# Performance work log

Hardware: AMD Instinct MI355X
Metric: run time of the kernel (lower is better)

## Reference

```python
import jax, jax.numpy as jnp
import numpy as np

B, T, I, U, O, BB = 256, 1024, 64, 256, 64, 128  # batch, seq, input, units, output, backbone_units

def lecun_tanh(x):
    return 1.7159 * jnp.tanh(0.666 * x)

def setup_inputs() -> dict:
    key = jax.random.key(0)
    ks = jax.random.split(key, 13)
    def lin(k, fan_in, fan_out):
        bound = 1.0 / np.sqrt(fan_in)
        kw, kb = jax.random.split(k)
        W = jax.random.uniform(kw, (fan_in, fan_out), jnp.float32, -bound, bound)
        b = jax.random.uniform(kb, (fan_out,), jnp.float32, -bound, bound)
        return W, b
    x = jax.random.normal(ks[0], (B, T, I), jnp.float32)
    W_bb, b_bb = lin(ks[1], I + U, BB)   # backbone Linear
    W_ff1, b_ff1 = lin(ks[2], BB, U)
    W_ff2, b_ff2 = lin(ks[3], BB, U)
    W_ta, b_ta = lin(ks[4], BB, U)       # time_a
    W_tb, b_tb = lin(ks[5], BB, U)       # time_b
    W_fc, b_fc = lin(ks[6], U, O)        # readout
    return {"x": x, "W_bb": W_bb, "b_bb": b_bb, "W_ff1": W_ff1, "b_ff1": b_ff1,
            "W_ff2": W_ff2, "b_ff2": b_ff2, "W_ta": W_ta, "b_ta": b_ta,
            "W_tb": W_tb, "b_tb": b_tb, "W_fc": W_fc, "b_fc": b_fc}

def reference(x, W_bb, b_bb, W_ff1, b_ff1, W_ff2, b_ff2, W_ta, b_ta, W_tb, b_tb, W_fc, b_fc):
    ts = jnp.float32(1.0)  # default elapsed time per step
    def step(h, xt):
        z = jnp.concatenate([xt, h], axis=-1)          # [B, I+U]
        g = lecun_tanh(z @ W_bb + b_bb)                # [B, BB]
        ff1 = jnp.tanh(g @ W_ff1 + b_ff1)              # [B, U]
        ff2 = jnp.tanh(g @ W_ff2 + b_ff2)
        t_interp = jax.nn.sigmoid((g @ W_ta + b_ta) * ts + (g @ W_tb + b_tb))
        h_new = ff1 * (1.0 - t_interp) + t_interp * ff2
        return h_new, h_new
    h0 = jnp.zeros((x.shape[0], U), x.dtype)
    h_last, hs = jax.lax.scan(step, h0, jnp.swapaxes(x, 0, 1))  # hs: [T, B, U]
    hs = jnp.swapaxes(hs, 0, 1)                                  # [B, T, U]
    out = hs @ W_fc + b_fc                                       # [B, T, O]
    return out, h_last
```

## Files before the change

### kernel.cpp

```cpp
#include <hip/hip_runtime.h>
#include <stdint.h>

#define B_ 256
#define T_ 1024
#define I_ 64
#define U_ 256
#define O_ 64
#define BB_ 128

typedef unsigned int u32;
typedef unsigned short u16;
typedef _Float16 half2_t __attribute__((ext_vector_type(2)));
typedef _Float16 f16x8 __attribute__((ext_vector_type(8)));
typedef float f32x4 __attribute__((ext_vector_type(4)));

#if defined(__has_builtin)
#if __has_builtin(__builtin_amdgcn_fdot2)
#define USE_DOT2 1
#else
#define USE_DOT2 0
#endif
#else
#define USE_DOT2 0
#endif

static __device__ __forceinline__ u32 packpair(float a, float b) {
  half2_t h; h.x = (_Float16)a; h.y = (_Float16)b;
  return __builtin_bit_cast(u32, h);
}
#if defined(__has_builtin) && __has_builtin(__builtin_amdgcn_cvt_pkrtz)
static __device__ __forceinline__ u32 pkrtz(float a, float b) {
  return __builtin_bit_cast(u32, __builtin_amdgcn_cvt_pkrtz(a, b));
}
#else
static __device__ __forceinline__ u32 pkrtz(float a, float b) {
  return packpair(a, b);
}
#endif
static __device__ __forceinline__ float unpack_lo(u32 u) {
  half2_t h = __builtin_bit_cast(half2_t, u); return (float)h.x;
}
static __device__ __forceinline__ float unpack_hi(u32 u) {
  half2_t h = __builtin_bit_cast(half2_t, u); return (float)h.y;
}
static __device__ __forceinline__ float dot2acc(u32 w, u32 z, float acc) {
#if USE_DOT2
  return __builtin_amdgcn_fdot2(__builtin_bit_cast(half2_t, w),
                                __builtin_bit_cast(half2_t, z), acc, false);
#else
  half2_t hw = __builtin_bit_cast(half2_t, w);
  half2_t hz = __builtin_bit_cast(half2_t, z);
  acc += (float)hw.x * (float)hz.x;
  acc += (float)hw.y * (float)hz.y;
  return acc;
#endif
}

template <int CTRL>
static __device__ __forceinline__ float dpp_mov_f(float v) {
  return __builtin_bit_cast(float, __builtin_amdgcn_update_dpp(
      0, __builtin_bit_cast(int, v), CTRL, 0xF, 0xF, true));
}
#define DPP_XOR1 0xB1
#define DPP_XOR2 0x4E
#define DPP_HMIR 0x141
#define DPP_MIRR 0x140

static __device__ __forceinline__ float fast_tanh(float x) {
  return 1.0f - 2.0f / (1.0f + __expf(2.0f * x));
}
static __device__ __forceinline__ float fast_sigmoid(float x) {
  return 1.0f / (1.0f + __expf(-x));
}

static __device__ __forceinline__ float rcpf(float x) {
#if defined(__has_builtin) && __has_builtin(__builtin_amdgcn_rcpf)
  return __builtin_amdgcn_rcpf(x);
#else
  return 1.0f / x;
#endif
}
static __device__ __forceinline__ float exp2fast(float x) {
#if defined(__has_builtin) && __has_builtin(__builtin_amdgcn_exp2f)
  return __builtin_amdgcn_exp2f(x);
#else
  return exp2f(x);
#endif
}

static __device__ __forceinline__ f32x4 mfma16(uint4 a, uint4 b, f32x4 c) {
  return __builtin_amdgcn_mfma_f32_16x16x32_f16(
      __builtin_bit_cast(f16x8, a), __builtin_bit_cast(f16x8, b), c, 0, 0, 0);
}

#define LOG2E 1.44269504f

__global__ __launch_bounds__(512, 2)
void px_kernel(const float* __restrict__ x,
               const float* __restrict__ W_bb, const float* __restrict__ b_bb,
               u32* __restrict__ Px)
{
  const int tid = threadIdx.x;
  const int l   = tid & 63;
  const int w   = tid >> 6;
  const int c16 = l & 15;
  const int q4  = l >> 4;
  const int rr  = blockIdx.x;
  const int t0  = blockIdx.y * 64;

  uint4 wpx[2];
  {
    const int colb = w * 16 + c16;
#pragma unroll
    for (int c = 0; c < 2; ++c) {
      u32 qv[4];
#pragma unroll
      for (int q = 0; q < 4; ++q) {
        const int k0 = c * 32 + q4 * 8 + 2 * q;
        qv[q] = packpair(W_bb[(size_t)k0 * BB_ + colb],
                         W_bb[(size_t)(k0 + 1) * BB_ + colb]);
      }
      wpx[c] = make_uint4(qv[0], qv[1], qv[2], qv[3]);
    }
  }
  const float bc = b_bb[w * 16 + c16];

  const float* xr = x + ((size_t)(rr * 16 + c16)) * T_ * I_ + q4 * 8;
  uint2* __restrict__ pxo =
      (uint2*)Px + ((size_t)rr * T_ + t0) * 512 + w * 64 + l;

  for (int i = 0; i < 64; ++i) {
    const int t = t0 + i;
    const float* xt = xr + (size_t)t * I_;
    float4 v0 = *(const float4*)(xt);
    float4 v1 = *(const float4*)(xt + 4);
    float4 v2 = *(const float4*)(xt + 32);
    float4 v3 = *(const float4*)(xt + 36);
    uint4 a0 = make_uint4(pkrtz(v0.x, v0.y), pkrtz(v0.z, v0.w),
                          pkrtz(v1.x, v1.y), pkrtz(v1.z, v1.w));
    uint4 a1 = make_uint4(pkrtz(v2.x, v2.y), pkrtz(v2.z, v2.w),
                          pkrtz(v3.x, v3.y), pkrtz(v3.z, v3.w));
    f32x4 acc = {bc, bc, bc, bc};
    acc = mfma16(a0, wpx[0], acc);
    acc = mfma16(a1, wpx[1], acc);
    uint2 o;
    o.x = pkrtz(acc[0], acc[1]);
    o.y = pkrtz(acc[2], acc[3]);
    pxo[(size_t)i * 512] = o;
  }
}

__global__ __launch_bounds__(512, 2)
void cfc_mfma2(const float* __restrict__ W_bb,
               const float* __restrict__ W_ff1, const float* __restrict__ b_ff1,
               const float* __restrict__ W_ff2, const float* __restrict__ b_ff2,
               const float* __restrict__ W_ta,  const float* __restrict__ b_ta,
               const float* __restrict__ W_tb,  const float* __restrict__ b_tb,
               float* __restrict__ out, u32* __restrict__ Hbuf,
               const u32* __restrict__ Px)
{
  __shared__ __align__(16) u32 s_z[2560];
  __shared__ __align__(16) u32 s_g[1024];

  const int tid = threadIdx.x;
  const int l   = tid & 63;
  const int w   = tid >> 6;
  const int c16 = l & 15;
  const int q4  = l >> 4;
  const int odd = l & 1;
  const int rr  = blockIdx.x;
  const int row0 = rr * 16;
  const int lx  = l ^ (l >> 4);

  uint4 wbb[8];
  {
    const int colb = w * 16 + c16;
#pragma unroll
    for (int c = 0; c < 8; ++c) {
      u32 qv[4];
#pragma unroll
      for (int q = 0; q < 4; ++q) {
        const int ulo = 32 * c + 4 * q4 + q;
        qv[q] = packpair(W_bb[(size_t)(64 + ulo) * BB_ + colb],
                         W_bb[(size_t)(80 + ulo) * BB_ + colb]);
      }
      wbb[c] = make_uint4(qv[0], qv[1], qv[2], qv[3]);
    }
  }
  uint4 wff[3][2][4];
#pragma unroll
  for (int ut = 0; ut < 2; ++ut) {
    const int u = w * 32 + ut * 16 + c16;
#pragma unroll
    for (int c = 0; c < 4; ++c) {
      u32 qa[4], qb[4], qc[4];
#pragma unroll
      for (int q = 0; q < 4; ++q) {
        const int k0 = c * 32 + q4 * 8 + 2 * q;
        const size_t i0 = (size_t)k0 * U_ + u, i1 = i0 + U_;
        qa[q] = packpair(W_ff1[i0], W_ff1[i1]);
        qb[q] = packpair(W_ff2[i0], W_ff2[i1]);
        qc[q] = packpair(W_ta[i0] + W_tb[i0], W_ta[i1] + W_tb[i1]);
      }
      wff[0][ut][c] = make_uint4(qa[0], qa[1], qa[2], qa[3]);
      wff[1][ut][c] = make_uint4(qb[0], qb[1], qb[2], qb[3]);
      wff[2][ut][c] = make_uint4(qc[0], qc[1], qc[2], qc[3]);
    }
  }

  float b1s[2], b2s[2], btn[2];
#pragma unroll
  for (int ut = 0; ut < 2; ++ut) {
    const int u = w * 32 + ut * 16 + c16;
    b1s[ut] = b_ff1[u] * (2.0f * LOG2E);
    b2s[ut] = b_ff2[u] * (2.0f * LOG2E);
    btn[ut] = -(b_ta[u] + b_tb[u]) * LOG2E;
  }

  const uint2* pxp = (const uint2*)Px + (size_t)rr * T_ * 512 + w * 64 + l;

  const int pg = w * 8 + (c16 >> 1);
  const int gw0 = ((pg >> 4) * 64 + 16 * ((pg >> 2) & 3)) * 4 + (pg & 3)
                  + 16 * q4 + (odd ? 8 : 0);

  int zws_[4];
#pragma unroll
  for (int r = 0; r < 4; ++r) {
    const int lane_cons = 4 * q4 + r + 16 * (c16 >> 2);
    const int LB = (2 + w) * 64 + lane_cons;
    const int SB = LB ^ (c16 >> 2);
    zws_[r] = SB * 4 + (c16 & 3);
  }
  u32* hp_[4];
#pragma unroll
  for (int r = 0; r < 4; ++r)
    hp_[r] = Hbuf + (size_t)(row0 + 4 * q4 + r) * T_ * 128 + (w * 16 + c16);

  reinterpret_cast<uint4*>(s_z)[128 + tid] = make_uint4(0u, 0u, 0u, 0u);
  uint2 pxc = pxp[0];
  __syncthreads();

  const uint4* z4 = (const uint4*)s_z;
  const uint4* g4 = (const uint4*)s_g;

  u32 hold0 = 0, hold1 = 0, hold2 = 0, hold3 = 0;

  for (int t = 0; t < T_; ++t) {
    uint2 pxn;
    const bool more = (t + 1 < T_);
    if (more) pxn = pxp[(size_t)(t + 1) * 512];

    f32x4 aA = {unpack_lo(pxc.x), unpack_hi(pxc.x),
                unpack_lo(pxc.y), unpack_hi(pxc.y)};
    f32x4 aB = {0.f, 0.f, 0.f, 0.f};
    aA = mfma16(z4[2 * 64 + lx], wbb[0], aA);
    aB = mfma16(z4[3 * 64 + lx], wbb[1], aB);
    aA = mfma16(z4[4 * 64 + lx], wbb[2], aA);
    aB = mfma16(z4[5 * 64 + lx], wbb[3], aB);
    aA = mfma16(z4[6 * 64 + lx], wbb[4], aA);
    aB = mfma16(z4[7 * 64 + lx], wbb[5], aB);
    aA = mfma16(z4[8 * 64 + lx], wbb[6], aA);
    aB = mfma16(z4[9 * 64 + lx], wbb[7], aB);
    const f32x4 ab = aA + aB;

    u32 gq[4];
#pragma unroll
    for (int r = 0; r < 4; ++r) {
      const float a  = ab[r] * (1.332f * LOG2E);
      const float rv = rcpf(exp2fast(a) + 1.0f);
      const float g  = __builtin_fmaf(rv, -3.4318f, 1.7159f);
      const float gp = dpp_mov_f<DPP_XOR1>(g);
      gq[r] = odd ? pkrtz(gp, g) : pkrtz(g, gp);
    }
    s_g[gw0]     = odd ? gq[2] : gq[0];
    s_g[gw0 + 4] = odd ? gq[3] : gq[1];
    __syncthreads();

    if (t) {
      const size_t o = (size_t)(t - 1) * 128;
      hp_[0][o] = hold0; hp_[1][o] = hold1;
      hp_[2][o] = hold2; hp_[3][o] = hold3;
    }

    f32x4 af[3][2];
#pragma unroll
    for (int mt = 0; mt < 3; ++mt)
#pragma unroll
      for (int ut = 0; ut < 2; ++ut)
        af[mt][ut] = (f32x4){0.f, 0.f, 0.f, 0.f};
#pragma unroll
    for (int c = 0; c < 4; ++c) {
      const uint4 ga = g4[c * 64 + l];
#pragma unroll
      for (int mt = 0; mt < 3; ++mt)
#pragma unroll
        for (int ut = 0; ut < 2; ++ut)
          af[mt][ut] = mfma16(ga, wff[mt][ut][c], af[mt][ut]);
    }

    u32 pk0, pk1, pk2, pk3;
#pragma unroll
    for (int r = 0; r < 4; ++r) {
      float h01[2];
#pragma unroll
      for (int ut = 0; ut < 2; ++ut) {
        const float E1 = exp2fast(__builtin_fmaf(af[0][ut][r], 2.0f * LOG2E, b1s[ut]));
        const float E2 = exp2fast(__builtin_fmaf(af[1][ut][r], 2.0f * LOG2E, b2s[ut]));
        const float E3 = exp2fast(__builtin_fmaf(af[2][ut][r], -LOG2E, btn[ut]));
        const float p2 = E2 + 1.0f, p3 = E3 + 1.0f;
        const float qq = p2 * p3;
        const float D  = __builtin_fmaf(E1, qq, qq);
        const float R  = rcpf(D);
        const float u2 = (E2 - E1) - qq;
        h01[ut] = __builtin_fmaf(R + R, u2, 1.0f);
      }
      const u32 pkv = pkrtz(h01[0], h01[1]);
      s_z[zws_[r]] = pkv;
      if (r == 0) pk0 = pkv; else if (r == 1) pk1 = pkv;
      else if (r == 2) pk2 = pkv; else pk3 = pkv;
    }
    hold0 = pk0; hold1 = pk1; hold2 = pk2; hold3 = pk3;
    pxc = pxn;
    __syncthreads();
  }

  {
    const size_t o = (size_t)(T_ - 1) * 128;
    hp_[0][o] = hold0; hp_[1][o] = hold1;
    hp_[2][o] = hold2; hp_[3][o] = hold3;
  }

  {
    const int c  = tid >> 6;
    const int tl = tid & 63;
    const uint4 hv = z4[(2 + c) * 64 + (tl ^ (tl >> 4))];
    const int row = row0 + (tl & 15);
    const int ub  = 32 * c + 4 * (tl >> 4);
    float* tail = out + (size_t)B_ * T_ * O_ + (size_t)row * 256;
#pragma unroll
    for (int q = 0; q < 4; ++q) {
      const u32 hp = (q == 0) ? hv.x : (q == 1) ? hv.y : (q == 2) ? hv.z : hv.w;
      tail[ub + q]      = unpack_lo(hp);
      tail[ub + q + 16] = unpack_hi(hp);
    }
  }
}

template <bool PX>
__global__ __launch_bounds__(512, 2)
void cfc_mfma(const float* __restrict__ x,
              const float* __restrict__ W_bb, const float* __restrict__ b_bb,
              const float* __restrict__ W_ff1, const float* __restrict__ b_ff1,
              const float* __restrict__ W_ff2, const float* __restrict__ b_ff2,
              const float* __restrict__ W_ta,  const float* __restrict__ b_ta,
              const float* __restrict__ W_tb,  const float* __restrict__ b_tb,
              float* __restrict__ out, u32* __restrict__ Hbuf,
              const u32* __restrict__ Px)
{
  __shared__ __align__(16) u32 s_z[2560];
  __shared__ __align__(16) u32 s_g[1024];

  const int tid = threadIdx.x;
  const int l   = tid & 63;
  const int w   = tid >> 6;
  const int c16 = l & 15;
  const int q4  = l >> 4;
  const int odd = l & 1;
  const int rr  = blockIdx.x;
  const int row0 = rr * 16;

  const int NBB = PX ? 8 : 10;
  const int KOFF = PX ? 64 : 0;
  uint4 wbb[10];
  {
    const int colb = w * 16 + c16;
    for (int c = 0; c < NBB; ++c) {
      u32 qv[4];
#pragma unroll
      for (int q = 0; q < 4; ++q) {
        const int k0 = KOFF + c * 32 + q4 * 8 + 2 * q;
        qv[q] = packpair(W_bb[(size_t)k0 * BB_ + colb],
                         W_bb[(size_t)(k0 + 1) * BB_ + colb]);
      }
      wbb[c] = make_uint4(qv[0], qv[1], qv[2], qv[3]);
    }
  }
  uint4 wff[3][2][4];
#pragma unroll
  for (int ut = 0; ut < 2; ++ut) {
    const int u = w * 32 + ut * 16 + c16;
#pragma unroll
    for (int c = 0; c < 4; ++c) {
      u32 qa[4], qb[4], qc[4];
#pragma unroll
      for (int q = 0; q < 4; ++q) {
        const int k0 = c * 32 + q4 * 8 + 2 * q;
        const size_t i0 = (size_t)k0 * U_ + u, i1 = i0 + U_;
        qa[q] = packpair(W_ff1[i0], W_ff1[i1]);
        qb[q] = packpair(W_ff2[i0], W_ff2[i1]);
        qc[q] = packpair(W_ta[i0] + W_tb[i0], W_ta[i1] + W_tb[i1]);
      }
      wff[0][ut][c] = make_uint4(qa[0], qa[1], qa[2], qa[3]);
      wff[1][ut][c] = make_uint4(qb[0], qb[1], qb[2], qb[3]);
      wff[2][ut][c] = make_uint4(qc[0], qc[1], qc[2], qc[3]);
    }
  }

  const float bgs = PX ? 0.f : b_bb[w * 16 + c16] * (1.332f * LOG2E);
  float b1s[2], b2s[2], btn[2];
#pragma unroll
  for (int ut = 0; ut < 2; ++ut) {
    const int u = w * 32 + ut * 16 + c16;
    b1s[ut] = b_ff1[u] * (2.0f * LOG2E);
    b2s[ut] = b_ff2[u] * (2.0f * LOG2E);
    btn[ut] = -(b_ta[u] + b_tb[u]) * LOG2E;
  }

  const int mx = tid >> 5, px_ = tid & 31;
  const float* xptr = x + (size_t)(row0 + mx) * T_ * I_ + 2 * px_;
  const int zxw = ((px_ >> 4) * 64 + mx + 16 * ((px_ >> 2) & 3)) * 4 + (px_ & 3);

  const uint2* pxp = (const uint2*)Px + (size_t)rr * T_ * 512 + w * 64 + l;

  const int rbase = odd ? 2 : 0;
  const int m0 = q4 * 4 + rbase, m1 = m0 + 1;
  const int pg = w * 8 + (c16 >> 1);
  const int gw0 = ((pg >> 4) * 64 + 16 * ((pg >> 2) & 3)) * 4 + (pg & 3)
                  + 16 * q4 + (odd ? 8 : 0);
  int zw_[2]; size_t hb0_[2], hb1_[2];
#pragma unroll
  for (int ut = 0; ut < 2; ++ut) {
    const int pu = w * 16 + ut * 8 + (c16 >> 1);
    zw_[ut] = ((2 + (pu >> 4)) * 64 + 16 * ((pu >> 2) & 3)) * 4 + (pu & 3)
              + 16 * q4 + (odd ? 8 : 0);
    hb0_[ut] = (size_t)(row0 + m0) * T_ * 128 + pu;
    hb1_[ut] = (size_t)(row0 + m1) * T_ * 128 + pu;
  }

  reinterpret_cast<uint4*>(s_z)[128 + tid] = make_uint4(0u, 0u, 0u, 0u);
  uint2 pxc;
  if (PX) {
    pxc = pxp[0];
  } else {
    __syncthreads();
    float2 xv = *(const float2*)xptr;
    s_z[zxw] = packpair(xv.x, xv.y);
  }
  __syncthreads();

  const uint4* z4 = (const uint4*)s_z;
  const uint4* g4 = (const uint4*)s_g;

  for (int t = 0; t < T_; ++t) {
    uint2 pxn;
    float2 xv;
    const bool more = (t + 1 < T_);
    if (PX) { if (more) pxn = pxp[(size_t)(t + 1) * 512]; }
    else    { if (more) xv = *(const float2*)(xptr + (size_t)(t + 1) * I_); }

    f32x4 aA, aB = {0.f, 0.f, 0.f, 0.f};
    if (PX) {
      aA = (f32x4){unpack_lo(pxc.x), unpack_hi(pxc.x),
                   unpack_lo(pxc.y), unpack_hi(pxc.y)};
      aA = mfma16(z4[2 * 64 + l], wbb[0], aA);
      aB = mfma16(z4[3 * 64 + l], wbb[1], aB);
      aA = mfma16(z4[4 * 64 + l], wbb[2], aA);
      aB = mfma16(z4[5 * 64 + l], wbb[3], aB);
      aA = mfma16(z4[6 * 64 + l], wbb[4], aA);
      aB = mfma16(z4[7 * 64 + l], wbb[5], aB);
      aA = mfma16(z4[8 * 64 + l], wbb[6], aA);
      aB = mfma16(z4[9 * 64 + l], wbb[7], aB);
    } else {
      aA = (f32x4){0.f, 0.f, 0.f, 0.f};
#pragma unroll
      for (int c = 0; c < 10; c += 2) {
        aA = mfma16(z4[c * 64 + l],       wbb[c],     aA);
        aB = mfma16(z4[(c + 1) * 64 + l], wbb[c + 1], aB);
      }
    }
    const f32x4 ab = aA + aB;

    u32 gq[4];
#pragma unroll
    for (int r = 0; r < 4; ++r) {
      const float a  = __builtin_fmaf(ab[r], 1.332f * LOG2E, bgs);
      const float rv = rcpf(exp2fast(a) + 1.0f);
      const float g  = __builtin_fmaf(rv, -3.4318f, 1.7159f);
      const float gp = dpp_mov_f<DPP_XOR1>(g);
      gq[r] = odd ? packpair(gp, g) : packpair(g, gp);
    }
    s_g[gw0]     = odd ? gq[2] : gq[0];
    s_g[gw0 + 4] = odd ? gq[3] : gq[1];
    __syncthreads();

    f32x4 af[3][2];
#pragma unroll
    for (int mt = 0; mt < 3; ++mt)
#pragma unroll
      for (int ut = 0; ut < 2; ++ut)
        af[mt][ut] = (f32x4){0.f, 0.f, 0.f, 0.f};
#pragma unroll
    for (int c = 0; c < 4; ++c) {
      const uint4 ga = g4[c * 64 + l];
#pragma unroll
      for (int mt = 0; mt < 3; ++mt)
#pragma unroll
        for (int ut = 0; ut < 2; ++ut)
          af[mt][ut] = mfma16(ga, wff[mt][ut][c], af[mt][ut]);
    }

#pragma unroll
    for (int ut = 0; ut < 2; ++ut) {
      u32 hq[4];
#pragma unroll
      for (int r = 0; r < 4; ++r) {
        const float E1 = exp2fast(__builtin_fmaf(af[0][ut][r], 2.0f * LOG2E, b1s[ut]));
        const float E2 = exp2fast(__builtin_fmaf(af[1][ut][r], 2.0f * LOG2E, b2s[ut]));
        const float E3 = exp2fast(__builtin_fmaf(af[2][ut][r], -LOG2E, btn[ut]));
        const float p2 = E2 + 1.0f, p3 = E3 + 1.0f;
        const float qq = p2 * p3;
        const float D  = __builtin_fmaf(E1, qq, qq);
        const float R  = rcpf(D);
        const float u2 = (E2 - E1) - qq;
        const float h  = __builtin_fmaf(R + R, u2, 1.0f);
        const float hp = dpp_mov_f<DPP_XOR1>(h);
        hq[r] = odd ? packpair(hp, h) : packpair(h, hp);
      }
      const u32 s0 = odd ? hq[2] : hq[0];
      const u32 s1 = odd ? hq[3] : hq[1];
      s_z[zw_[ut]]     = s0;
      s_z[zw_[ut] + 4] = s1;
      Hbuf[hb0_[ut] + (size_t)t * 128] = s0;
      Hbuf[hb1_[ut] + (size_t)t * 128] = s1;
    }
    if (PX) { pxc = pxn; }
    else    { if (more) s_z[zxw] = packpair(xv.x, xv.y); }
    __syncthreads();
  }

  {
    const uint4 hv = reinterpret_cast<const uint4*>(s_z)[128 + tid];
    float2* tail = (float2*)(out + (size_t)B_ * T_ * O_);
#pragma unroll
    for (int i = 0; i < 4; ++i) {
      const int vh   = tid * 4 + i;
      const int ch   = vh >> 8;
      const int lane = (vh >> 2) & 63;
      const int slot = vh & 3;
      const int m    = lane & 15;
      const int bq   = lane >> 4;
      const int pu   = ch * 16 + bq * 4 + slot;
      const u32 hp   = (i == 0) ? hv.x : (i == 1) ? hv.y : (i == 2) ? hv.z : hv.w;
      float2 hf; hf.x = unpack_lo(hp); hf.y = unpack_hi(hp);
      tail[(size_t)(row0 + m) * 128 + pu] = hf;
    }
  }
}

template <bool DEFER>
__global__ __launch_bounds__(1024)
void cfc_kernel(const float* __restrict__ x,
                const float* __restrict__ W_bb, const float* __restrict__ b_bb,
                const float* __restrict__ W_ff1, const float* __restrict__ b_ff1,
                const float* __restrict__ W_ff2, const float* __restrict__ b_ff2,
                const float* __restrict__ W_ta,  const float* __restrict__ b_ta,
                const float* __restrict__ W_tb,  const float* __restrict__ b_tb,
                const float* __restrict__ W_fc,  const float* __restrict__ b_fc,
                float* __restrict__ out, u32* __restrict__ Hbuf)
{
  __shared__ __align__(16) u32 s_z2[160];
  __shared__ __align__(16) u32 s_g2[64];
  u16* s_gh = (u16*)s_g2;

  const int tid = threadIdx.x;
  const int r   = blockIdx.x;

  const int ca  = tid >> 3;
  const int kga = tid & 7;
  const int jb = tid >> 2;
  const int kq = tid & 3;
  const int ro = tid >> 4;
  const int rk = tid & 15;

  u32 wbb[20];
#pragma unroll
  for (int j = 0; j < 5; ++j)
#pragma unroll
    for (int q = 0; q < 4; ++q) {
      int p = 4 * (kga + 8 * j) + q;
      wbb[4 * j + q] = packpair(W_bb[(2 * p) * BB_ + ca],
                                W_bb[(2 * p + 1) * BB_ + ca]);
    }
  u32 wf1[16], wf2[16], wta[16], wtb[16];
#pragma unroll
  for (int j = 0; j < 4; ++j)
#pragma unroll
    for (int q = 0; q < 4; ++q) {
      int p = 4 * (kq + 4 * j) + q;
      int k0 = 2 * p, k1 = 2 * p + 1;
      wf1[4 * j + q] = packpair(W_ff1[k0 * U_ + jb], W_ff1[k1 * U_ + jb]);
      wf2[4 * j + q] = packpair(W_ff2[k0 * U_ + jb], W_ff2[k1 * U_ + jb]);
      wta[4 * j + q] = packpair(W_ta [k0 * U_ + jb], W_ta [k1 * U_ + jb]);
      wtb[4 * j + q] = packpair(W_tb [k0 * U_ + jb], W_tb [k1 * U_ + jb]);
    }
  u32 wfc[8];
  float bfo = 0.f;
  if (!DEFER) {
#pragma unroll
    for (int j = 0; j < 2; ++j)
#pragma unroll
      for (int q = 0; q < 4; ++q) {
        int p = 4 * (rk + 16 * j) + q;
        wfc[4 * j + q] = packpair(W_fc[(2 * p) * O_ + ro],
                                  W_fc[(2 * p + 1) * O_ + ro]);
      }
    bfo = b_fc[ro];
  }
  const float bbbc = b_bb[ca];
  const float b1 = b_ff1[jb], b2 = b_ff2[jb];
  const float bta = b_ta[jb], btb = b_tb[jb];

  const float* xrow = x + (size_t)r * T_ * I_;
  const size_t out_row = (size_t)r * T_ * O_;
  u32* __restrict__ hrow = DEFER ? (Hbuf + (size_t)r * T_ * (U_ / 2)) : nullptr;

  if (tid < 160) s_z2[tid] = 0u;
  __syncthreads();
  if (tid < 32) {
    float2 xv = ((const float2*)xrow)[tid];
    s_z2[tid] = packpair(xv.x, xv.y);
  }
  __syncthreads();

  for (int t = 0; t < T_; ++t) {
    float2 xv;
    const bool ldx = (tid < 32) && (t + 1 < T_);
    if (ldx) xv = ((const float2*)(xrow + (size_t)(t + 1) * I_))[tid];

    float bacc = 0.f;
#pragma unroll
    for (int j = 0; j < 5; ++j) {
      uint4 zz = *reinterpret_cast<const uint4*>(s_z2 + 4 * (kga + 8 * j));
      bacc = dot2acc(wbb[4 * j + 0], zz.x, bacc);
      bacc = dot2acc(wbb[4 * j + 1], zz.y, bacc);
      bacc = dot2acc(wbb[4 * j + 2], zz.z, bacc);
      bacc = dot2acc(wbb[4 * j + 3], zz.w, bacc);
    }
    bacc += dpp_mov_f<DPP_XOR1>(bacc);
    bacc += dpp_mov_f<DPP_XOR2>(bacc);
    bacc += dpp_mov_f<DPP_HMIR>(bacc);
    float g = 1.7159f * fast_tanh(0.666f * (bacc + bbbc));

    float racc = 0.f;
    if (!DEFER) {
#pragma unroll
      for (int j = 0; j < 2; ++j) {
        uint4 hh = *reinterpret_cast<const uint4*>(s_z2 + 32 + 4 * (rk + 16 * j));
        racc = dot2acc(wfc[4 * j + 0], hh.x, racc);
        racc = dot2acc(wfc[4 * j + 1], hh.y, racc);
        racc = dot2acc(wfc[4 * j + 2], hh.z, racc);
        racc = dot2acc(wfc[4 * j + 3], hh.w, racc);
      }
      racc += dpp_mov_f<DPP_XOR1>(racc);
      racc += dpp_mov_f<DPP_XOR2>(racc);
      racc += dpp_mov_f<DPP_HMIR>(racc);
      racc += dpp_mov_f<DPP_MIRR>(racc);
    }
    if ((tid & 7) == 0)
      s_gh[ca] = __builtin_bit_cast(u16, (_Float16)g);
    if (!DEFER && t > 0 && rk == 0)
      out[out_row + (size_t)(t - 1) * O_ + ro] = racc + bfo;
    __syncthreads();

    float a1 = 0.f, a2 = 0.f, a3 = 0.f, a4 = 0.f;
#pragma unroll
    for (int j = 0; j < 4; ++j) {
      uint4 gg = *reinterpret_cast<const uint4*>(s_g2 + 4 * (kq + 4 * j));
      a1 = dot2acc(wf1[4 * j + 0], gg.x, a1);
      a1 = dot2acc(wf1[4 * j + 1], gg.y, a1);
      a1 = dot2acc(wf1[4 * j + 2], gg.z, a1);
      a1 = dot2acc(wf1[4 * j + 3], gg.w, a1);
      a2 = dot2acc(wf2[4 * j + 0], gg.x, a2);
      a2 = dot2acc(wf2[4 * j + 1], gg.y, a2);
      a2 = dot2acc(wf2[4 * j + 2], gg.z, a2);
      a2 = dot2acc(wf2[4 * j + 3], gg.w, a2);
      a3 = dot2acc(wta[4 * j + 0], gg.x, a3);
      a3 = dot2acc(wta[4 * j + 1], gg.y, a3);
      a3 = dot2acc(wta[4 * j + 2], gg.z, a3);
      a3 = dot2acc(wta[4 * j + 3], gg.w, a3);
      a4 = dot2acc(wtb[4 * j + 0], gg.x, a4);
      a4 = dot2acc(wtb[4 * j + 1], gg.y, a4);
      a4 = dot2acc(wtb[4 * j + 2], gg.z, a4);
      a4 = dot2acc(wtb[4 * j + 3], gg.w, a4);
    }
    a1 += dpp_mov_f<DPP_XOR1>(a1); a1 += dpp_mov_f<DPP_XOR2>(a1);
    a2 += dpp_mov_f<DPP_XOR1>(a2); a2 += dpp_mov_f<DPP_XOR2>(a2);
    a3 += dpp_mov_f<DPP_XOR1>(a3); a3 += dpp_mov_f<DPP_XOR2>(a3);
    a4 += dpp_mov_f<DPP_XOR1>(a4); a4 += dpp_mov_f<DPP_XOR2>(a4);
    float f1 = fast_tanh(a1 + b1);
    float f2 = fast_tanh(a2 + b2);
    float ti = fast_sigmoid(a3 + bta + a4 + btb);
    float h  = f1 + ti * (f2 - f1);
    float hq = dpp_mov_f<DPP_HMIR>(h);

    if ((tid & 7) == 0) {
      u32 pr = packpair(h, hq);
      int m = tid >> 3;
      s_z2[32 + m] = pr;
      if (DEFER) hrow[(size_t)t * (U_ / 2) + m] = pr;
    }
    if (ldx) s_z2[tid] = packpair(xv.x, xv.y);
    __syncthreads();
  }

  if (!DEFER) {
    float racc = 0.f;
#pragma unroll
    for (int j = 0; j < 2; ++j) {
      uint4 hh = *reinterpret_cast<const uint4*>(s_z2 + 32 + 4 * (rk + 16 * j));
      racc = dot2acc(wfc[4 * j + 0], hh.x, racc);
      racc = dot2acc(wfc[4 * j + 1], hh.y, racc);
      racc = dot2acc(wfc[4 * j + 2], hh.z, racc);
      racc = dot2acc(wfc[4 * j + 3], hh.w, racc);
    }
    racc += dpp_mov_f<DPP_XOR1>(racc);
    racc += dpp_mov_f<DPP_XOR2>(racc);
    racc += dpp_mov_f<DPP_HMIR>(racc);
    racc += dpp_mov_f<DPP_MIRR>(racc);
    if (rk == 0)
      out[out_row + (size_t)(T_ - 1) * O_ + ro] = racc + bfo;
  }

  if (tid < 128) {
    u32 hp = s_z2[32 + tid];
    float2 hv; hv.x = unpack_lo(hp); hv.y = unpack_hi(hp);
    ((float2*)(out + (size_t)B_ * T_ * O_))[r * 128 + tid] = hv;
  }
}

template <bool NEWPAIR>
__global__ __launch_bounds__(512)
void ro_kernel(const u32* __restrict__ Hbuf,
               const float* __restrict__ W_fc, const float* __restrict__ b_fc,
               float* __restrict__ out)
{
  __shared__ __align__(16) u32 s_h[8 * 128];
  const int tid = threadIdx.x;
  const int o   = tid & 63;
  const int w   = tid >> 6;
  const int r   = blockIdx.x;

  u32 wfc[128];
#pragma unroll
  for (int p = 0; p < 128; ++p) {
    if (NEWPAIR) {
      const int ulo = 32 * (p >> 4) + (p & 15);
      wfc[p] = packpair(W_fc[(size_t)ulo * O_ + o],
                        W_fc[(size_t)(ulo + 16) * O_ + o]);
    } else {
      wfc[p] = packpair(W_fc[(2 * p) * O_ + o], W_fc[(2 * p + 1) * O_ + o]);
    }
  }
  const float bo = b_fc[o];

  const u32* hrow = Hbuf + (size_t)r * T_ * 128;
  const size_t out_row = (size_t)r * T_ * O_;

  for (int c = 0; c < T_ / 8; ++c) {
    *(uint2*)(s_h + 2 * tid) =
        *(const uint2*)(hrow + (size_t)c * 1024 + 2 * tid);
    __syncthreads();
    float acc = bo;
    const uint4* h4 = reinterpret_cast<const uint4*>(s_h + w * 128);
#pragma unroll
    for (int i = 0; i < 32; ++i) {
      uint4 hh = h4[i];
      acc = dot2acc(wfc[4 * i + 0], hh.x, acc);
      acc = dot2acc(wfc[4 * i + 1], hh.y, acc);
      acc = dot2acc(wfc[4 * i + 2], hh.z, acc);
      acc = dot2acc(wfc[4 * i + 3], hh.w, acc);
    }
    out[out_row + (size_t)(8 * c + w) * O_ + o] = acc;
    __syncthreads();
  }
}

extern "C" void kernel_launch(void* const* d_in, const int* in_sizes, int n_in,
                              void* d_out, int out_size, void* d_ws, size_t ws_size,
                              hipStream_t stream) {
  const float* x     = (const float*)d_in[0];
  const float* W_bb  = (const float*)d_in[1];
  const float* b_bb  = (const float*)d_in[2];
  const float* W_ff1 = (const float*)d_in[3];
  const float* b_ff1 = (const float*)d_in[4];
  const float* W_ff2 = (const float*)d_in[5];
  const float* b_ff2 = (const float*)d_in[6];
  const float* W_ta  = (const float*)d_in[7];
  const float* b_ta  = (const float*)d_in[8];
  const float* W_tb  = (const float*)d_in[9];
  const float* b_tb  = (const float*)d_in[10];
  const float* W_fc  = (const float*)d_in[11];
  const float* b_fc  = (const float*)d_in[12];
  float* out = (float*)d_out;

  const size_t h_bytes  = (size_t)B_ * T_ * (U_ / 2) * sizeof(u32);
  const size_t px_bytes = (size_t)B_ * T_ * (BB_ / 2) * sizeof(u32);
  if (ws_size >= h_bytes + px_bytes) {
    u32* Hbuf = (u32*)d_ws;
    u32* Px   = (u32*)((char*)d_ws + h_bytes);
    px_kernel<<<dim3(16, T_ / 64), dim3(512), 0, stream>>>(x, W_bb, b_bb, Px);
    cfc_mfma2<<<dim3(B_ / 16), dim3(512), 0, stream>>>(
        W_bb, W_ff1, b_ff1, W_ff2, b_ff2,
        W_ta, b_ta, W_tb, b_tb, out, Hbuf, Px);
    ro_kernel<true><<<dim3(B_), dim3(512), 0, stream>>>(Hbuf, W_fc, b_fc, out);
  } else if (ws_size >= h_bytes) {
    u32* Hbuf = (u32*)d_ws;
    cfc_mfma<false><<<dim3(B_ / 16), dim3(512), 0, stream>>>(
        x, W_bb, b_bb, W_ff1, b_ff1, W_ff2, b_ff2,
        W_ta, b_ta, W_tb, b_tb, out, Hbuf, nullptr);
    ro_kernel<false><<<dim3(B_), dim3(512), 0, stream>>>(Hbuf, W_fc, b_fc, out);
  } else {
    cfc_kernel<false><<<dim3(B_), dim3(1024), 0, stream>>>(
        x, W_bb, b_bb, W_ff1, b_ff1, W_ff2, b_ff2,
        W_ta, b_ta, W_tb, b_tb, W_fc, b_fc, out, nullptr);
  }
}
```

Measured before the change: 1.649 ms.

## Process two independent 16-row batch tiles per block to interleave recurrent chains

The recurrent kernel now handles 32 batch rows per block as two independent 16-row chains (A and B) sharing the register-resident weights. Each step issues both chains' MFMAs and activations between the same barriers, so one chain's dependency latency can overlap the other's work. The backbone MFMA accumulation is also split into four partial accumulators instead of two, shortening the dependent chain. The grid halves to 8 blocks, which reduces CU occupancy, and per-thread register and LDS use rise, so per-step latency may increase.

```diff
diff --git a/kernel.cpp b/kernel.cpp
--- a/kernel.cpp
+++ b/kernel.cpp
@@ -151,16 +151,18 @@
 }
 
 __global__ __launch_bounds__(512, 2)
-void cfc_mfma2(const float* __restrict__ W_bb,
-               const float* __restrict__ W_ff1, const float* __restrict__ b_ff1,
-               const float* __restrict__ W_ff2, const float* __restrict__ b_ff2,
-               const float* __restrict__ W_ta,  const float* __restrict__ b_ta,
-               const float* __restrict__ W_tb,  const float* __restrict__ b_tb,
-               float* __restrict__ out, u32* __restrict__ Hbuf,
-               const u32* __restrict__ Px)
+void cfc_dual(const float* __restrict__ W_bb,
+              const float* __restrict__ W_ff1, const float* __restrict__ b_ff1,
+              const float* __restrict__ W_ff2, const float* __restrict__ b_ff2,
+              const float* __restrict__ W_ta,  const float* __restrict__ b_ta,
+              const float* __restrict__ W_tb,  const float* __restrict__ b_tb,
+              float* __restrict__ out, u32* __restrict__ Hbuf,
+              const u32* __restrict__ Px)
 {
-  __shared__ __align__(16) u32 s_z[2560];
-  __shared__ __align__(16) u32 s_g[1024];
+  __shared__ __align__(16) u32 s_zA[2048];
+  __shared__ __align__(16) u32 s_zB[2048];
+  __shared__ __align__(16) u32 s_gA[1024];
+  __shared__ __align__(16) u32 s_gB[1024];
 
   const int tid = threadIdx.x;
   const int l   = tid & 63;
@@ -169,7 +171,8 @@
   const int q4  = l >> 4;
   const int odd = l & 1;
   const int rr  = blockIdx.x;
-  const int row0 = rr * 16;
+  const int row0A = rr * 32;
+  const int row0B = rr * 32 + 16;
   const int lx  = l ^ (l >> 4);
 
   uint4 wbb[8];
@@ -217,7 +220,8 @@
     btn[ut] = -(b_ta[u] + b_tb[u]) * LOG2E;
   }
 
-  const uint2* pxp = (const uint2*)Px + (size_t)rr * T_ * 512 + w * 64 + l;
+  const uint2* pxpA = (const uint2*)Px + (size_t)(2 * rr) * T_ * 512 + w * 64 + l;
+  const uint2* pxpB = pxpA + (size_t)T_ * 512;
 
   const int pg = w * 8 + (c16 >> 1);
   const int gw0 = ((pg >> 4) * 64 + 16 * ((pg >> 2) & 3)) * 4 + (pg & 3)
@@ -227,86 +231,142 @@
 #pragma unroll
   for (int r = 0; r < 4; ++r) {
     const int lane_cons = 4 * q4 + r + 16 * (c16 >> 2);
-    const int LB = (2 + w) * 64 + lane_cons;
+    const int LB = w * 64 + lane_cons;
     const int SB = LB ^ (c16 >> 2);
     zws_[r] = SB * 4 + (c16 & 3);
   }
-  u32* hp_[4];
-#pragma unroll
-  for (int r = 0; r < 4; ++r)
-    hp_[r] = Hbuf + (size_t)(row0 + 4 * q4 + r) * T_ * 128 + (w * 16 + c16);
-
-  reinterpret_cast<uint4*>(s_z)[128 + tid] = make_uint4(0u, 0u, 0u, 0u);
-  uint2 pxc = pxp[0];
+  u32 *hpA_[4], *hpB_[4];
+#pragma unroll
+  for (int r = 0; r < 4; ++r) {
+    hpA_[r] = Hbuf + (size_t)(row0A + 4 * q4 + r) * T_ * 128 + (w * 16 + c16);
+    hpB_[r] = Hbuf + (size_t)(row0B + 4 * q4 + r) * T_ * 128 + (w * 16 + c16);
+  }
+
+  reinterpret_cast<uint4*>(s_zA)[tid] = make_uint4(0u, 0u, 0u, 0u);
+  reinterpret_cast<uint4*>(s_zB)[tid] = make_uint4(0u, 0u, 0u, 0u);
+  uint2 pxcA = pxpA[0];
+  uint2 pxcB = pxpB[0];
   __syncthreads();
 
-  const uint4* z4 = (const uint4*)s_z;
-  const uint4* g4 = (const uint4*)s_g;
-
-  u32 hold0 = 0, hold1 = 0, hold2 = 0, hold3 = 0;
+  const uint4* zA = (const uint4*)s_zA;
+  const uint4* zB = (const uint4*)s_zB;
+  const uint4* gA4 = (const uint4*)s_gA;
+  const uint4* gB4 = (const uint4*)s_gB;
+
+  u32 hA0 = 0, hA1 = 0, hA2 = 0, hA3 = 0;
+  u32 hB0 = 0, hB1 = 0, hB2 = 0, hB3 = 0;
 
   for (int t = 0; t < T_; ++t) {
-    uint2 pxn;
+    uint2 pxnA, pxnB;
     const bool more = (t + 1 < T_);
-    if (more) pxn = pxp[(size_t)(t + 1) * 512];
-
-    f32x4 aA = {unpack_lo(pxc.x), unpack_hi(pxc.x),
-                unpack_lo(pxc.y), unpack_hi(pxc.y)};
-    f32x4 aB = {0.f, 0.f, 0.f, 0.f};
-    aA = mfma16(z4[2 * 64 + lx], wbb[0], aA);
-    aB = mfma16(z4[3 * 64 + lx], wbb[1], aB);
-    aA = mfma16(z4[4 * 64 + lx], wbb[2], aA);
-    aB = mfma16(z4[5 * 64 + lx], wbb[3], aB);
-    aA = mfma16(z4[6 * 64 + lx], wbb[4], aA);
-    aB = mfma16(z4[7 * 64 + lx], wbb[5], aB);
-    aA = mfma16(z4[8 * 64 + lx], wbb[6], aA);
-    aB = mfma16(z4[9 * 64 + lx], wbb[7], aB);
-    const f32x4 ab = aA + aB;
-
-    u32 gq[4];
-#pragma unroll
-    for (int r = 0; r < 4; ++r) {
-      const float a  = ab[r] * (1.332f * LOG2E);
-      const float rv = rcpf(exp2fast(a) + 1.0f);
-      const float g  = __builtin_fmaf(rv, -3.4318f, 1.7159f);
-      const float gp = dpp_mov_f<DPP_XOR1>(g);
-      gq[r] = odd ? pkrtz(gp, g) : pkrtz(g, gp);
-    }
-    s_g[gw0]     = odd ? gq[2] : gq[0];
-    s_g[gw0 + 4] = odd ? gq[3] : gq[1];
+    if (more) {
+      pxnA = pxpA[(size_t)(t + 1) * 512];
+      pxnB = pxpB[(size_t)(t + 1) * 512];
+    }
+
+    f32x4 a0 = {unpack_lo(pxcA.x), unpack_hi(pxcA.x),
+                unpack_lo(pxcA.y), unpack_hi(pxcA.y)};
+    f32x4 a1 = {0.f, 0.f, 0.f, 0.f};
+    f32x4 a2 = {0.f, 0.f, 0.f, 0.f};
+    f32x4 a3 = {0.f, 0.f, 0.f, 0.f};
+    a0 = mfma16(zA[0 * 64 + lx], wbb[0], a0);
+    a1 = mfma16(zA[1 * 64 + lx], wbb[1], a1);
+    a2 = mfma16(zA[2 * 64 + lx], wbb[2], a2);
+    a3 = mfma16(zA[3 * 64 + lx], wbb[3], a3);
+    a0 = mfma16(zA[4 * 64 + lx], wbb[4], a0);
+    a1 = mfma16(zA[5 * 64 + lx], wbb[5], a1);
+    a2 = mfma16(zA[6 * 64 + lx], wbb[6], a2);
+    a3 = mfma16(zA[7 * 64 + lx], wbb[7], a3);
+    const f32x4 abA = (a0 + a1) + (a2 + a3);
+
+    f32x4 c0 = {unpack_lo(pxcB.x), unpack_hi(pxcB.x),
+                unpack_lo(pxcB.y), unpack_hi(pxcB.y)};
+    f32x4 c1 = {0.f, 0.f, 0.f, 0.f};
+    f32x4 c2 = {0.f, 0.f, 0.f, 0.f};
+    f32x4 c3 = {0.f, 0.f, 0.f, 0.f};
+    c0 = mfma16(zB[0 * 64 + lx], wbb[0], c0);
+    c1 = mfma16(zB[1 * 64 + lx], wbb[1], c1);
+    c2 = mfma16(zB[2 * 64 + lx], wbb[2], c2);
+    c3 = mfma16(zB[3 * 64 + lx], wbb[3], c3);
+    c0 = mfma16(zB[4 * 64 + lx], wbb[4], c0);
+    c1 = mfma16(zB[5 * 64 + lx], wbb[5], c1);
+    c2 = mfma16(zB[6 * 64 + lx], wbb[6], c2);
+    c3 = mfma16(zB[7 * 64 + lx], wbb[7], c3);
+    const f32x4 abB = (c0 + c1) + (c2 + c3);
+
+    {
+      u32 gq[4];
+#pragma unroll
+      for (int r = 0; r < 4; ++r) {
+        const float a  = abA[r] * (1.332f * LOG2E);
+        const float rv = rcpf(exp2fast(a) + 1.0f);
+        const float g  = __builtin_fmaf(rv, -3.4318f, 1.7159f);
+        const float gp = dpp_mov_f<DPP_XOR1>(g);
+        gq[r] = odd ? pkrtz(gp, g) : pkrtz(g, gp);
+      }
+      s_gA[gw0]     = odd ? gq[2] : gq[0];
+      s_gA[gw0 + 4] = odd ? gq[3] : gq[1];
+    }
+    {
+      u32 gq[4];
+#pragma unroll
+      for (int r = 0; r < 4; ++r) {
+        const float a  = abB[r] * (1.332f * LOG2E);
+        const float rv = rcpf(exp2fast(a) + 1.0f);
+        const float g  = __builtin_fmaf(rv, -3.4318f, 1.7159f);
+        const float gp = dpp_mov_f<DPP_XOR1>(g);
+        gq[r] = odd ? pkrtz(gp, g) : pkrtz(g, gp);
+      }
+      s_gB[gw0]     = odd ? gq[2] : gq[0];
+      s_gB[gw0 + 4] = odd ? gq[3] : gq[1];
+    }
     __syncthreads();
 
     if (t) {
       const size_t o = (size_t)(t - 1) * 128;
-      hp_[0][o] = hold0; hp_[1][o] = hold1;
-      hp_[2][o] = hold2; hp_[3][o] = hold3;
-    }
-
-    f32x4 af[3][2];
+      hpA_[0][o] = hA0; hpA_[1][o] = hA1; hpA_[2][o] = hA2; hpA_[3][o] = hA3;
+      hpB_[0][o] = hB0; hpB_[1][o] = hB1; hpB_[2][o] = hB2; hpB_[3][o] = hB3;
+    }
+
+    f32x4 afA[3][2];
 #pragma unroll
     for (int mt = 0; mt < 3; ++mt)
 #pragma unroll
       for (int ut = 0; ut < 2; ++ut)
-        af[mt][ut] = (f32x4){0.f, 0.f, 0.f, 0.f};
+        afA[mt][ut] = (f32x4){0.f, 0.f, 0.f, 0.f};
 #pragma unroll
     for (int c = 0; c < 4; ++c) {
-      const uint4 ga = g4[c * 64 + l];
+      const uint4 ga = gA4[c * 64 + l];
 #pragma unroll
       for (int mt = 0; mt < 3; ++mt)
 #pragma unroll
         for (int ut = 0; ut < 2; ++ut)
-          af[mt][ut] = mfma16(ga, wff[mt][ut][c], af[mt][ut]);
-    }
-
-    u32 pk0, pk1, pk2, pk3;
+          afA[mt][ut] = mfma16(ga, wff[mt][ut][c], afA[mt][ut]);
+    }
+    f32x4 afB[3][2];
+#pragma unroll
+    for (int mt = 0; mt < 3; ++mt)
+#pragma unroll
+      for (int ut = 0; ut < 2; ++ut)
+        afB[mt][ut] = (f32x4){0.f, 0.f, 0.f, 0.f};
+#pragma unroll
+    for (int c = 0; c < 4; ++c) {
+      const uint4 ga = gB4[c * 64 + l];
+#pragma unroll
+      for (int mt = 0; mt < 3; ++mt)
+#pragma unroll
+        for (int ut = 0; ut < 2; ++ut)
+          afB[mt][ut] = mfma16(ga, wff[mt][ut][c], afB[mt][ut]);
+    }
+
 #pragma unroll
     for (int r = 0; r < 4; ++r) {
       float h01[2];
 #pragma unroll
       for (int ut = 0; ut < 2; ++ut) {
-        const float E1 = exp2fast(__builtin_fmaf(af[0][ut][r], 2.0f * LOG2E, b1s[ut]));
-        const float E2 = exp2fast(__builtin_fmaf(af[1][ut][r], 2.0f * LOG2E, b2s[ut]));
-        const float E3 = exp2fast(__builtin_fmaf(af[2][ut][r], -LOG2E, btn[ut]));
+        const float E1 = exp2fast(__builtin_fmaf(afA[0][ut][r], 2.0f * LOG2E, b1s[ut]));
+        const float E2 = exp2fast(__builtin_fmaf(afA[1][ut][r], 2.0f * LOG2E, b2s[ut]));
+        const float E3 = exp2fast(__builtin_fmaf(afA[2][ut][r], -LOG2E, btn[ut]));
         const float p2 = E2 + 1.0f, p3 = E3 + 1.0f;
         const float qq = p2 * p3;
         const float D  = __builtin_fmaf(E1, qq, qq);
@@ -315,33 +375,65 @@
         h01[ut] = __builtin_fmaf(R + R, u2, 1.0f);
       }
       const u32 pkv = pkrtz(h01[0], h01[1]);
-      s_z[zws_[r]] = pkv;
-      if (r == 0) pk0 = pkv; else if (r == 1) pk1 = pkv;
-      else if (r == 2) pk2 = pkv; else pk3 = pkv;
-    }
-    hold0 = pk0; hold1 = pk1; hold2 = pk2; hold3 = pk3;
-    pxc = pxn;
+      s_zA[zws_[r]] = pkv;
+      if (r == 0) hA0 = pkv; else if (r == 1) hA1 = pkv;
+      else if (r == 2) hA2 = pkv; else hA3 = pkv;
+    }
+#pragma unroll
+    for (int r = 0; r < 4; ++r) {
+      float h01[2];
+#pragma unroll
+      for (int ut = 0; ut < 2; ++ut) {
+        const float E1 = exp2fast(__builtin_fmaf(afB[0][ut][r], 2.0f * LOG2E, b1s[ut]));
+        const float E2 = exp2fast(__builtin_fmaf(afB[1][ut][r], 2.0f * LOG2E, b2s[ut]));
+        const float E3 = exp2fast(__builtin_fmaf(afB[2][ut][r], -LOG2E, btn[ut]));
+        const float p2 = E2 + 1.0f, p3 = E3 + 1.0f;
+        const float qq = p2 * p3;
+        const float D  = __builtin_fmaf(E1, qq, qq);
+        const float R  = rcpf(D);
+        const float u2 = (E2 - E1) - qq;
+        h01[ut] = __builtin_fmaf(R + R, u2, 1.0f);
+      }
+      const u32 pkv = pkrtz(h01[0], h01[1]);
+      s_zB[zws_[r]] = pkv;
+      if (r == 0) hB0 = pkv; else if (r == 1) hB1 = pkv;
+      else if (r == 2) hB2 = pkv; else hB3 = pkv;
+    }
+    pxcA = pxnA;
+    pxcB = pxnB;
     __syncthreads();
   }
 
   {
     const size_t o = (size_t)(T_ - 1) * 128;
-    hp_[0][o] = hold0; hp_[1][o] = hold1;
-    hp_[2][o] = hold2; hp_[3][o] = hold3;
+    hpA_[0][o] = hA0; hpA_[1][o] = hA1; hpA_[2][o] = hA2; hpA_[3][o] = hA3;
+    hpB_[0][o] = hB0; hpB_[1][o] = hB1; hpB_[2][o] = hB2; hpB_[3][o] = hB3;
   }
 
   {
     const int c  = tid >> 6;
     const int tl = tid & 63;
-    const uint4 hv = z4[(2 + c) * 64 + (tl ^ (tl >> 4))];
-    const int row = row0 + (tl & 15);
+    const int tlx = tl ^ (tl >> 4);
     const int ub  = 32 * c + 4 * (tl >> 4);
-    float* tail = out + (size_t)B_ * T_ * O_ + (size_t)row * 256;
-#pragma unroll
-    for (int q = 0; q < 4; ++q) {
-      const u32 hp = (q == 0) ? hv.x : (q == 1) ? hv.y : (q == 2) ? hv.z : hv.w;
-      tail[ub + q]      = unpack_lo(hp);
-      tail[ub + q + 16] = unpack_hi(hp);
+    {
+      const uint4 hv = zA[c * 64 + tlx];
+      float* tail = out + (size_t)B_ * T_ * O_ + (size_t)(row0A + (tl & 15)) * 256;
+#pragma unroll
+      for (int q = 0; q < 4; ++q) {
+        const u32 hp = (q == 0) ? hv.x : (q == 1) ? hv.y : (q == 2) ? hv.z : hv.w;
+        tail[ub + q]      = unpack_lo(hp);
+        tail[ub + q + 16] = unpack_hi(hp);
+      }
+    }
+    {
+      const uint4 hv = zB[c * 64 + tlx];
+      float* tail = out + (size_t)B_ * T_ * O_ + (size_t)(row0B + (tl & 15)) * 256;
+#pragma unroll
+      for (int q = 0; q < 4; ++q) {
+        const u32 hp = (q == 0) ? hv.x : (q == 1) ? hv.y : (q == 2) ? hv.z : hv.w;
+        tail[ub + q]      = unpack_lo(hp);
+        tail[ub + q + 16] = unpack_hi(hp);
+      }
     }
   }
 }
@@ -809,7 +901,7 @@
     u32* Hbuf = (u32*)d_ws;
     u32* Px   = (u32*)((char*)d_ws + h_bytes);
     px_kernel<<<dim3(16, T_ / 64), dim3(512), 0, stream>>>(x, W_bb, b_bb, Px);
-    cfc_mfma2<<<dim3(B_ / 16), dim3(512), 0, stream>>>(
+    cfc_dual<<<dim3(B_ / 32), dim3(512), 0, stream>>>(
         W_bb, W_ff1, b_ff1, W_ff2, b_ff2,
         W_ta, b_ta, W_tb, b_tb, out, Hbuf, Px);
     ro_kernel<true><<<dim3(B_), dim3(512), 0, stream>>>(Hbuf, W_fc, b_fc, out);
```

Measured after the change: 3.084 ms. 87.0% more time.
